# Performance work log

Hardware: AMD Instinct MI355X
Metric: run time of the kernel (lower is better)

The kernel has to match this reference:

```python
import jax, jax.numpy as jnp
import numpy as np

HEADS = 10
HEAD_DIM = 64
ATTN_SCALE = HEAD_DIM ** -0.5
SHARED_SCORE_SHIFT = 0.6931472  # ln(2)
SHARED_SCORE_SCALE = 1.0
EPS = 1e-5


def expand_first(feat, scale=1.0):
    # feat: [b, ...]; broadcast style stats from batch 0 and b//2 over each half
    b = feat.shape[0]
    style = jnp.stack([feat[0], feat[b // 2]])[:, None]          # [2, 1, ...]
    style = jnp.broadcast_to(style, (2, b // 2) + feat.shape[1:])
    if scale != 1.0:
        factors = jnp.where(jnp.arange(b // 2) == 0, 1.0, scale)
        factors = factors.reshape((1, b // 2) + (1,) * (feat.ndim - 1))
        style = style * factors
    return style.reshape(feat.shape)


def adain(feat):
    # stats over the sequence axis (dim=-2); torch .var() is unbiased (ddof=1)
    mean = jnp.mean(feat, axis=-2, keepdims=True)
    std = jnp.sqrt(jnp.var(feat, axis=-2, keepdims=True, ddof=1) + EPS)
    style_mean = expand_first(mean)
    style_std = expand_first(std)
    return (feat - mean) / std * style_std + style_mean


def setup_inputs() -> dict:
    key = jax.random.key(0)
    B, N, C = 4, 2048, 640
    ks = jax.random.split(key, 6)
    hidden_states = jax.random.normal(ks[0], (B, N, C), dtype=jnp.float32)
    w_scale = 0.03
    wq = jax.random.normal(ks[1], (C, C), dtype=jnp.float32) * w_scale
    wk = jax.random.normal(ks[2], (C, C), dtype=jnp.float32) * w_scale
    wv = jax.random.normal(ks[3], (C, C), dtype=jnp.float32) * w_scale
    wo = jax.random.normal(ks[4], (C, C), dtype=jnp.float32) * w_scale
    bo = jnp.zeros((C,), dtype=jnp.float32)
    return {"hidden_states": hidden_states, "wq": wq, "wk": wk, "wv": wv, "wo": wo, "bo": bo}


def reference(hidden_states, wq, wk, wv, wo, bo):
    b, n, c = hidden_states.shape
    # to_q / to_k / to_v (bias-free Linear: y = x @ W^T)
    q = hidden_states @ wq.T
    k = hidden_states @ wk.T
    v = hidden_states @ wv.T
    # [b, heads, n, head_dim]
    q = q.reshape(b, n, HEADS, HEAD_DIM).transpose(0, 2, 1, 3)
    k = k.reshape(b, n, HEADS, HEAD_DIM).transpose(0, 2, 1, 3)
    v = v.reshape(b, n, HEADS, HEAD_DIM).transpose(0, 2, 1, 3)
    # AdaIN on queries and keys (adain_values=False)
    q = adain(q)
    k = adain(k)
    # cross-batch KV style sharing
    k = expand_first(k, SHARED_SCORE_SCALE)
    v = expand_first(v, SHARED_SCORE_SCALE)
    # shifted scaled-dot-product attention: shift added to logit columns >= Nq
    logits = jnp.einsum('bhqd,bhkd->bhqk', q, k) * ATTN_SCALE
    nq, nk = q.shape[2], k.shape[2]
    shift = SHARED_SCORE_SHIFT * (jnp.arange(nk) >= nq).astype(logits.dtype)
    logits = logits + shift  # no-op here since nk == nq, kept for fidelity
    probs = jax.nn.softmax(logits, axis=-1)
    out = jnp.einsum('bhqk,bhkd->bhqd', probs, v)
    # merge heads, output projection (to_out[0] Linear + to_out[1] Dropout=identity)
    out = out.transpose(0, 2, 1, 3).reshape(b, n, HEADS * HEAD_DIM)
    out = out @ wo.T + bo
    # residual connection, rescale_output_factor = 1
    return out + hidden_states
```

## Files before the change

kernel.cpp:

```cpp
#include <hip/hip_runtime.h>
#include <hip/hip_bf16.h>
#include <math.h>

#define Bb 4
#define Nn 2048
#define Cc 640
#define Hh 10
#define Dd 64
#define EPSf 1e-5f
#define QSCALE 0.18033688f
#define KVT 64

typedef __attribute__((ext_vector_type(8))) short bf16x8;
typedef __attribute__((ext_vector_type(4))) float f32x4;
typedef __attribute__((ext_vector_type(16))) float f32x16;
typedef __attribute__((ext_vector_type(8))) unsigned short u16x8;
typedef __attribute__((ext_vector_type(4))) unsigned int u32x4;
typedef __attribute__((ext_vector_type(2))) unsigned int u32x2v;

__device__ inline unsigned short f2bf(float f) {
    unsigned int x = __float_as_uint(f);
    unsigned int r = (x + 0x7fffu + ((x >> 16) & 1u)) >> 16;
    return (unsigned short)r;
}
__device__ inline float bf2f(unsigned short v) {
    return __uint_as_float(((unsigned int)v) << 16);
}
__device__ inline unsigned pkbf(float a, float b) {
    __hip_bfloat162 t = __float22bfloat162_rn(float2{a, b});
    union { __hip_bfloat162 h; unsigned u; } cv; cv.h = t;
    return cv.u;
}
__device__ inline unsigned cvtpk(float lo, float hi) {
    unsigned r;
    asm("v_cvt_pk_bf16_f32 %0, %1, %2" : "=v"(r) : "v"(lo), "v"(hi));
    return r;
}
__device__ inline f32x4 mfma16(bf16x8 a, bf16x8 b, f32x4 c) {
    return __builtin_amdgcn_mfma_f32_16x16x32_bf16(a, b, c, 0, 0, 0);
}
__device__ inline f32x16 mfma32(bf16x8 a, bf16x8 b, f32x16 c) {
    return __builtin_amdgcn_mfma_f32_32x32x16_bf16(a, b, c, 0, 0, 0);
}
__device__ inline void gl16(const ushort* g, char* l) {
    __builtin_amdgcn_global_load_lds(
        (const __attribute__((address_space(1))) unsigned int*)g,
        (__attribute__((address_space(3))) unsigned int*)l, 16, 0, 0);
}

__global__ __launch_bounds__(256)
void tobf16_all(const float* __restrict__ hs, const float* __restrict__ wq,
                const float* __restrict__ wk, const float* __restrict__ wv,
                const float* __restrict__ wo,
                ushort* __restrict__ Xb, ushort* __restrict__ Wqb,
                ushort* __restrict__ Wkb, ushort* __restrict__ Wvb,
                ushort* __restrict__ Wob) {
    const int bid = blockIdx.x;
    const float* src;
    ushort* dst;
    int i;
    if (bid < 2560) {
        src = hs; dst = Xb; i = bid * 256 + threadIdx.x;
    } else {
        int w = (bid - 2560) / 200;
        int rb = (bid - 2560) % 200;
        src = (w == 0) ? wq : (w == 1) ? wk : (w == 2) ? wv : wo;
        dst = (w == 0) ? Wqb : (w == 1) ? Wkb : (w == 2) ? Wvb : Wob;
        i = rb * 256 + threadIdx.x;
    }
    const size_t base = (size_t)i * 8;
    float4 a = *reinterpret_cast<const float4*>(src + base);
    float4 b = *reinterpret_cast<const float4*>(src + base + 4);
    u16x8 o;
    o[0] = f2bf(a.x); o[1] = f2bf(a.y); o[2] = f2bf(a.z); o[3] = f2bf(a.w);
    o[4] = f2bf(b.x); o[5] = f2bf(b.y); o[6] = f2bf(b.z); o[7] = f2bf(b.w);
    *reinterpret_cast<u16x8*>(dst + base) = o;
}

template<int MODE>
__device__ __forceinline__ void gemm_body(
    const ushort* __restrict__ X, const ushort* __restrict__ W,
    ushort* __restrict__ outh, float* __restrict__ outf,
    const float* __restrict__ bo, const ushort* __restrict__ hsb,
    float* __restrict__ Pstats,
    int mt, int h, char* As, char* Bs)
{
    const int tid = threadIdx.x;
    const int wv = tid >> 6, lane = tid & 63;
    const int c = lane & 15, g = lane >> 4;
    const int r0 = mt * 128;
    const int xr0 = (MODE == 1 || MODE == 2) ? (r0 < Nn ? r0 : r0 + Nn) : r0;
    const int o0 = h * 64;

    const int grow = lane >> 3;
    const int gcol = ((((lane & 7) * 16) ^ ((lane >> 3) << 4)) >> 1);

    f32x4 acc[2][4];
    #pragma unroll
    for (int i = 0; i < 2; ++i)
        #pragma unroll
        for (int j = 0; j < 4; ++j)
            acc[i][j] = (f32x4){0.f, 0.f, 0.f, 0.f};

    for (int k0 = 0; k0 < Cc; k0 += 64) {
        __syncthreads();
        #pragma unroll
        for (int i = 0; i < 4; ++i) {
            int a = wv * 4 + i;
            gl16(X + (size_t)(xr0 + a * 8 + grow) * Cc + k0 + gcol, As + a * 1024);
        }
        #pragma unroll
        for (int i = 0; i < 2; ++i) {
            int bb = wv * 2 + i;
            gl16(W + (size_t)(o0 + bb * 8 + grow) * Cc + k0 + gcol, Bs + bb * 1024);
        }
        __syncthreads();

        bf16x8 xf[2][2], wf[4][2];
        #pragma unroll
        for (int rt = 0; rt < 2; ++rt) {
            int row = wv * 32 + rt * 16 + c;
            #pragma unroll
            for (int ks = 0; ks < 2; ++ks)
                xf[rt][ks] = *reinterpret_cast<const bf16x8*>(
                    As + row * 128 + ((ks * 64 + g * 16) ^ ((row & 7) << 4)));
        }
        #pragma unroll
        for (int ct = 0; ct < 4; ++ct) {
            int row = ct * 16 + c;
            #pragma unroll
            for (int ks = 0; ks < 2; ++ks)
                wf[ct][ks] = *reinterpret_cast<const bf16x8*>(
                    Bs + row * 128 + ((ks * 64 + g * 16) ^ ((row & 7) << 4)));
        }
        #pragma unroll
        for (int rt = 0; rt < 2; ++rt)
            #pragma unroll
            for (int ct = 0; ct < 4; ++ct)
                #pragma unroll
                for (int ks = 0; ks < 2; ++ks) {
                    if constexpr (MODE == 2)
                        acc[rt][ct] = mfma16(xf[rt][ks], wf[ct][ks], acc[rt][ct]);
                    else
                        acc[rt][ct] = mfma16(wf[ct][ks], xf[rt][ks], acc[rt][ct]);
                }
    }

    if constexpr (MODE == 0 || MODE == 1) {
        #pragma unroll
        for (int rt = 0; rt < 2; ++rt) {
            int r = r0 + wv * 32 + rt * 16 + c;
            int bi = r >> 11, n = r & 2047;
            #pragma unroll
            for (int ct = 0; ct < 4; ++ct) {
                int d0 = ct * 16 + g * 4;
                ushort4 v4;
                v4.x = f2bf(acc[rt][ct][0]); v4.y = f2bf(acc[rt][ct][1]);
                v4.z = f2bf(acc[rt][ct][2]); v4.w = f2bf(acc[rt][ct][3]);
                *reinterpret_cast<ushort4*>(&outh[(((size_t)(bi * Hh + h)) * Nn + n) * Dd + d0]) = v4;
            }
        }
    } else if constexpr (MODE == 2) {
        #pragma unroll
        for (int rt = 0; rt < 2; ++rt) {
            int r = r0 + wv * 32 + rt * 16 + g * 4;
            int kb = r >> 11, n = r & 2047;
            #pragma unroll
            for (int ct = 0; ct < 4; ++ct) {
                int d = ct * 16 + c;
                ushort4 v4;
                v4.x = f2bf(acc[rt][ct][0]); v4.y = f2bf(acc[rt][ct][1]);
                v4.z = f2bf(acc[rt][ct][2]); v4.w = f2bf(acc[rt][ct][3]);
                *reinterpret_cast<ushort4*>(&outh[(((size_t)(kb * Hh + h)) * Dd + d) * Nn + n]) = v4;
            }
        }
    } else {
        #pragma unroll
        for (int rt = 0; rt < 2; ++rt) {
            int r = r0 + wv * 32 + rt * 16 + c;
            #pragma unroll
            for (int ct = 0; ct < 4; ++ct) {
                int o = h * 64 + ct * 16 + g * 4;
                float4 bvv = *reinterpret_cast<const float4*>(&bo[o]);
                ushort4 hv4 = *reinterpret_cast<const ushort4*>(&hsb[(size_t)r * Cc + o]);
                float4 ov;
                ov.x = acc[rt][ct][0] + bvv.x + bf2f(hv4.x);
                ov.y = acc[rt][ct][1] + bvv.y + bf2f(hv4.y);
                ov.z = acc[rt][ct][2] + bvv.z + bf2f(hv4.z);
                ov.w = acc[rt][ct][3] + bvv.w + bf2f(hv4.w);
                *reinterpret_cast<float4*>(&outf[(size_t)r * Cc + o]) = ov;
            }
        }
    }

    if constexpr (MODE == 0) {
        __syncthreads();
        float* Sw  = (float*)As;
        float* Sw2 = (float*)(As + 1024);
        #pragma unroll
        for (int ct = 0; ct < 4; ++ct) {
            #pragma unroll
            for (int rg = 0; rg < 4; ++rg) {
                float a0 = acc[0][ct][rg], a1 = acc[1][ct][rg];
                float v = a0 + a1;
                float q = a0 * a0 + a1 * a1;
                #pragma unroll
                for (int m = 1; m < 16; m <<= 1) {
                    v += __shfl_xor(v, m);
                    q += __shfl_xor(q, m);
                }
                if (c == 0) {
                    int d = ct * 16 + g * 4 + rg;
                    Sw[wv * 64 + d] = v;
                    Sw2[wv * 64 + d] = q;
                }
            }
        }
        __syncthreads();
        if (tid < 64) {
            float s = Sw[tid] + Sw[64 + tid] + Sw[128 + tid] + Sw[192 + tid];
            float q = Sw2[tid] + Sw2[64 + tid] + Sw2[128 + tid] + Sw2[192 + tid];
            int bi = mt >> 4, slot = mt & 15;
            int bh = bi * Hh + h;
            float* p = Pstats + ((size_t)(bh * 16 + slot) * 2) * 64;
            p[tid] = s;
            p[64 + tid] = q;
        }
    }
}

__global__ __launch_bounds__(256)
void gemm_qkv(const ushort* __restrict__ X, const ushort* __restrict__ Wq,
              const ushort* __restrict__ Wk, const ushort* __restrict__ Wv,
              ushort* __restrict__ Qh, ushort* __restrict__ K16,
              ushort* __restrict__ Vt16, float* __restrict__ Pstats) {
    __shared__ alignas(16) char As[16384];
    __shared__ alignas(16) char Bs[8192];
    const int bx = blockIdx.x;
    if (bx < 64)
        gemm_body<0>(X, Wq, Qh, nullptr, nullptr, nullptr, Pstats, bx, blockIdx.y, As, Bs);
    else if (bx < 96)
        gemm_body<1>(X, Wk, K16, nullptr, nullptr, nullptr, nullptr, bx - 64, blockIdx.y, As, Bs);
    else
        gemm_body<2>(X, Wv, Vt16, nullptr, nullptr, nullptr, nullptr, bx - 96, blockIdx.y, As, Bs);
}

__global__ __launch_bounds__(256)
void gemm_out(const ushort* __restrict__ Ain, const ushort* __restrict__ Wo,
              float* __restrict__ out, const float* __restrict__ bo,
              const ushort* __restrict__ hsb) {
    __shared__ alignas(16) char As[16384];
    __shared__ alignas(16) char Bs[8192];
    gemm_body<3>(Ain, Wo, nullptr, out, bo, hsb, nullptr, blockIdx.x, blockIdx.y, As, Bs);
}

__global__ __launch_bounds__(512, 4)
void attn_mfma(const ushort* __restrict__ Qh, const float* __restrict__ Pstats,
               const ushort* __restrict__ Kb, const ushort* __restrict__ Vtb,
               ushort* __restrict__ Ao) {
    __shared__ alignas(16) char smem[32768];
    __shared__ float lsh[8][32];
    __shared__ float statl[4][64];

    const int tid = threadIdx.x;
    const int wid = tid >> 6, lane = tid & 63;
    const int half = wid >> 2, wq = wid & 3;
    const int q31 = lane & 31, hi = lane >> 5;
    const int bh = blockIdx.x, b = bh / Hh, h = bh % Hh, kb = b >> 1;
    const int qw0 = blockIdx.y * 128 + wq * 32;
    const int kv0 = half * (Nn / 2);

    char* Ksh = smem + half * 8192;
    char* Vsh = smem + 16384 + half * 8192;

    const ushort* qp = Qh + ((size_t)bh * Nn + qw0) * Dd;
    const ushort* kp = Kb + ((size_t)(kb * Hh + h) * Nn + kv0) * Dd;
    const ushort* vp = Vtb + ((size_t)(kb * Hh + h)) * Dd * Nn + kv0;

    if (b & 1) {
        if (tid < 128) {
            const int which = tid >> 6;
            const int d = tid & 63;
            const int tb = which ? (bh - Hh) : bh;
            const float* p = Pstats + ((size_t)(tb * 16) * 2) * 64;
            float s = 0.f, q = 0.f;
            #pragma unroll
            for (int j = 0; j < 16; ++j) {
                s += p[(j * 2) * 64 + d];
                q += p[(j * 2 + 1) * 64 + d];
            }
            float mu = s / (float)Nn;
            float var = (q - (float)Nn * mu * mu) / (float)(Nn - 1);
            float sd = sqrtf(var + EPSf);
            statl[which * 2 + 0][d] = mu;
            statl[which * 2 + 1][d] = sd;
        }
        __syncthreads();
    }

    bf16x8 qf[4];
    #pragma unroll
    for (int dsl = 0; dsl < 4; ++dsl) {
        const int d0 = dsl * 16 + hi * 8;
        u16x8 qin = *reinterpret_cast<const u16x8*>(qp + (size_t)q31 * Dd + d0);
        float x[8];
        #pragma unroll
        for (int j = 0; j < 8; ++j) x[j] = bf2f(qin[j]);
        if (b & 1) {
            #pragma unroll
            for (int j = 0; j < 8; ++j) {
                float r = statl[3][d0 + j] / statl[1][d0 + j];
                x[j] = (x[j] * r + (statl[2][d0 + j] - statl[0][d0 + j] * r)) * QSCALE;
            }
        } else {
            #pragma unroll
            for (int j = 0; j < 8; ++j) x[j] *= QSCALE;
        }
        u32x4 pw = {pkbf(x[0], x[1]), pkbf(x[2], x[3]), pkbf(x[4], x[5]), pkbf(x[6], x[7])};
        qf[dsl] = *reinterpret_cast<bf16x8*>(&pw);
    }

    f32x16 acc0, acc1;
    #pragma unroll
    for (int r = 0; r < 16; ++r) { acc0[r] = 0.f; acc1[r] = 0.f; }
    float l = 0.f;

    const int htid = tid & 255;
    const int srow = htid >> 3, sch = htid & 7;
    const int swz = (sch * 16) ^ ((srow & 7) << 4);
    const int soff0 = srow * 128 + swz;
    const int soff1 = (srow + 32) * 128 + swz;
    const ushort* kg0 = kp + (size_t)srow * Dd + sch * 8;
    const ushort* kg1 = kp + (size_t)(srow + 32) * Dd + sch * 8;
    const ushort* vg0 = vp + (size_t)srow * Nn + sch * 8;
    const ushort* vg1 = vp + (size_t)(srow + 32) * Nn + sch * 8;

    bf16x8 kr0 = *reinterpret_cast<const bf16x8*>(kg0);
    bf16x8 kr1 = *reinterpret_cast<const bf16x8*>(kg1);
    bf16x8 vr0 = *reinterpret_cast<const bf16x8*>(vg0);
    bf16x8 vr1 = *reinterpret_cast<const bf16x8*>(vg1);
    *reinterpret_cast<bf16x8*>(Ksh + soff0) = kr0;
    *reinterpret_cast<bf16x8*>(Ksh + soff1) = kr1;
    *reinterpret_cast<bf16x8*>(Vsh + soff0) = vr0;
    *reinterpret_cast<bf16x8*>(Vsh + soff1) = vr1;
    __syncthreads();

    const int kx = (q31 & 7) << 4;

    for (int kt = 0; kt < Nn / 2; kt += KVT) {
        const bool has_next = (kt + KVT) < (Nn / 2);
        if (has_next) {
            kr0 = *reinterpret_cast<const bf16x8*>(kg0 + (size_t)(kt + KVT) * Dd);
            kr1 = *reinterpret_cast<const bf16x8*>(kg1 + (size_t)(kt + KVT) * Dd);
            vr0 = *reinterpret_cast<const bf16x8*>(vg0 + kt + KVT);
            vr1 = *reinterpret_cast<const bf16x8*>(vg1 + kt + KVT);
        }

        f32x16 st0, st1;
        #pragma unroll
        for (int r = 0; r < 16; ++r) { st0[r] = 0.f; st1[r] = 0.f; }
        #pragma unroll
        for (int dsl = 0; dsl < 4; ++dsl) {
            bf16x8 kf0 = *reinterpret_cast<const bf16x8*>(
                Ksh + q31 * 128 + ((dsl * 32 + hi * 16) ^ kx));
            bf16x8 kf1 = *reinterpret_cast<const bf16x8*>(
                Ksh + (q31 + 32) * 128 + ((dsl * 32 + hi * 16) ^ kx));
            st0 = mfma32(kf0, qf[dsl], st0);
            st1 = mfma32(kf1, qf[dsl], st1);
        }

        #pragma unroll
        for (int r = 0; r < 16; ++r) st0[r] = __builtin_amdgcn_exp2f(st0[r]);
        #pragma unroll
        for (int r = 0; r < 16; ++r) st1[r] = __builtin_amdgcn_exp2f(st1[r]);

        {
            float s2[16];
            #pragma unroll
            for (int r = 0; r < 16; ++r) s2[r] = st0[r] + st1[r];
            float s4[8];
            #pragma unroll
            for (int r = 0; r < 8; ++r) s4[r] = s2[r] + s2[r + 8];
            float s8[4];
            #pragma unroll
            for (int r = 0; r < 4; ++r) s8[r] = s4[r] + s4[r + 4];
            l += (s8[0] + s8[1]) + (s8[2] + s8[3]);
        }

        #pragma unroll
        for (int kvm = 0; kvm < 2; ++kvm) {
            #pragma unroll
            for (int tt = 0; tt < 2; ++tt) {
                float p0, p1, p2, p3, p4, p5, p6, p7;
                if (kvm == 0) {
                    p0 = st0[8*tt+0]; p1 = st0[8*tt+1]; p2 = st0[8*tt+2]; p3 = st0[8*tt+3];
                    p4 = st0[8*tt+4]; p5 = st0[8*tt+5]; p6 = st0[8*tt+6]; p7 = st0[8*tt+7];
                } else {
                    p0 = st1[8*tt+0]; p1 = st1[8*tt+1]; p2 = st1[8*tt+2]; p3 = st1[8*tt+3];
                    p4 = st1[8*tt+4]; p5 = st1[8*tt+5]; p6 = st1[8*tt+6]; p7 = st1[8*tt+7];
                }
                unsigned a0 = cvtpk(p0, p1);
                unsigned a1 = cvtpk(p2, p3);
                unsigned b0 = cvtpk(p4, p5);
                unsigned b1 = cvtpk(p6, p7);
                u32x2v r0 = __builtin_amdgcn_permlane32_swap(a0, b0, false, false);
                u32x2v r1 = __builtin_amdgcn_permlane32_swap(a1, b1, false, false);
                u32x4 fw = {r0[0], r1[0], r0[1], r1[1]};
                bf16x8 pf = *reinterpret_cast<bf16x8*>(&fw);
                const int km = kvm * 2 + tt;
                bf16x8 vf0 = *reinterpret_cast<const bf16x8*>(
                    Vsh + q31 * 128 + ((km * 32 + hi * 16) ^ kx));
                bf16x8 vf1 = *reinterpret_cast<const bf16x8*>(
                    Vsh + (q31 + 32) * 128 + ((km * 32 + hi * 16) ^ kx));
                acc0 = mfma32(pf, vf0, acc0);
                acc1 = mfma32(pf, vf1, acc1);
            }
        }

        if (has_next) {
            __syncthreads();
            *reinterpret_cast<bf16x8*>(Ksh + soff0) = kr0;
            *reinterpret_cast<bf16x8*>(Ksh + soff1) = kr1;
            *reinterpret_cast<bf16x8*>(Vsh + soff0) = vr0;
            *reinterpret_cast<bf16x8*>(Vsh + soff1) = vr1;
            __syncthreads();
        }
    }

    l += __shfl_xor(l, 32);
    lsh[wid][q31] = l;
    __syncthreads();
    float* fs = (float*)smem;
    if (half == 1) {
        float* dst = fs + wq * 2048;
        #pragma unroll
        for (int r = 0; r < 16; ++r) {
            dst[r * 64 + lane] = acc0[r];
            dst[(16 + r) * 64 + lane] = acc1[r];
        }
    }
    __syncthreads();
    if (half == 0) {
        const float* src = fs + wq * 2048;
        float ltot = l + lsh[wid + 4][q31];
        float inv = 1.0f / ltot;
        #pragma unroll
        for (int r = 0; r < 16; ++r) {
            const int qlr = (r & 3) + 8 * (r >> 2) + 4 * hi;
            float o0 = (acc0[r] + src[r * 64 + lane]) * inv;
            float o1 = (acc1[r] + src[(16 + r) * 64 + lane]) * inv;
            size_t o = (size_t)(b * Nn + qw0 + qlr) * Cc + h * Dd + q31;
            Ao[o]      = f2bf(o0);
            Ao[o + 32] = f2bf(o1);
        }
    }
}

extern "C" void kernel_launch(void* const* d_in, const int* in_sizes, int n_in,
                              void* d_out, int out_size, void* d_ws, size_t ws_size,
                              hipStream_t stream) {
    const float* hs = (const float*)d_in[0];
    const float* wq = (const float*)d_in[1];
    const float* wk = (const float*)d_in[2];
    const float* wv = (const float*)d_in[3];
    const float* wo = (const float*)d_in[4];
    const float* bo = (const float*)d_in[5];
    float* out = (float*)d_out;

    ushort* Xb   = (ushort*)d_ws;
    ushort* Wqb  = Xb + 5242880;
    ushort* Wkb  = Wqb + 409600;
    ushort* Wvb  = Wkb + 409600;
    ushort* Wob  = Wvb + 409600;
    ushort* Qh   = Wob + 409600;
    ushort* K16  = Qh + 5242880;
    ushort* Vt16 = K16 + 2621440;
    ushort* Aob  = Vt16 + 2621440;
    float*  Pstats = (float*)(Aob + 5242880);

    tobf16_all<<<3360, 256, 0, stream>>>(hs, wq, wk, wv, wo, Xb, Wqb, Wkb, Wvb, Wob);

    gemm_qkv<<<dim3(128, 10), 256, 0, stream>>>(Xb, Wqb, Wkb, Wvb, Qh, K16, Vt16, Pstats);
    attn_mfma<<<dim3(40, 16), 512, 0, stream>>>(Qh, Pstats, K16, Vt16, Aob);
    gemm_out<<<dim3(64, 10), 256, 0, stream>>>(Aob, Wob, out, bo, Xb);
}
```

Baseline: 117.3 us.

## Double-buffer attention K/V tiles with direct global-to-LDS loads

Replaces the register-staged K/V prefetch in the attention kernel with a double-buffered LDS scheme that issues direct global-to-LDS loads (gl16) for the next tile while the current tile is computed. This cuts the per-iteration barriers from two to one and frees the registers that held the prefetched tiles. In exchange the kernel's shared memory doubles to 64 KB, which may limit how many blocks fit per CU under launch_bounds(512,4).

```diff
diff --git a/kernel.cpp b/kernel.cpp
--- a/kernel.cpp
+++ b/kernel.cpp
@@ -258,20 +258,18 @@
 void attn_mfma(const ushort* __restrict__ Qh, const float* __restrict__ Pstats,
                const ushort* __restrict__ Kb, const ushort* __restrict__ Vtb,
                ushort* __restrict__ Ao) {
-    __shared__ alignas(16) char smem[32768];
+    __shared__ alignas(16) char smem[65536];
     __shared__ float lsh[8][32];
     __shared__ float statl[4][64];
 
     const int tid = threadIdx.x;
     const int wid = tid >> 6, lane = tid & 63;
     const int half = wid >> 2, wq = wid & 3;
+    const int hw = wid & 3;
     const int q31 = lane & 31, hi = lane >> 5;
     const int bh = blockIdx.x, b = bh / Hh, h = bh % Hh, kb = b >> 1;
     const int qw0 = blockIdx.y * 128 + wq * 32;
     const int kv0 = half * (Nn / 2);
-
-    char* Ksh = smem + half * 8192;
-    char* Vsh = smem + 16384 + half * 8192;
 
     const ushort* qp = Qh + ((size_t)bh * Nn + qw0) * Dd;
     const ushort* kp = Kb + ((size_t)(kb * Hh + h) * Nn + kv0) * Dd;
@@ -325,36 +323,32 @@
     for (int r = 0; r < 16; ++r) { acc0[r] = 0.f; acc1[r] = 0.f; }
     float l = 0.f;
 
-    const int htid = tid & 255;
-    const int srow = htid >> 3, sch = htid & 7;
-    const int swz = (sch * 16) ^ ((srow & 7) << 4);
-    const int soff0 = srow * 128 + swz;
-    const int soff1 = (srow + 32) * 128 + swz;
-    const ushort* kg0 = kp + (size_t)srow * Dd + sch * 8;
-    const ushort* kg1 = kp + (size_t)(srow + 32) * Dd + sch * 8;
-    const ushort* vg0 = vp + (size_t)srow * Nn + sch * 8;
-    const ushort* vg1 = vp + (size_t)(srow + 32) * Nn + sch * 8;
-
-    bf16x8 kr0 = *reinterpret_cast<const bf16x8*>(kg0);
-    bf16x8 kr1 = *reinterpret_cast<const bf16x8*>(kg1);
-    bf16x8 vr0 = *reinterpret_cast<const bf16x8*>(vg0);
-    bf16x8 vr1 = *reinterpret_cast<const bf16x8*>(vg1);
-    *reinterpret_cast<bf16x8*>(Ksh + soff0) = kr0;
-    *reinterpret_cast<bf16x8*>(Ksh + soff1) = kr1;
-    *reinterpret_cast<bf16x8*>(Vsh + soff0) = vr0;
-    *reinterpret_cast<bf16x8*>(Vsh + soff1) = vr1;
+    const int grow = lane >> 3;
+    const int gcolE = ((((lane & 7) * 16) ^ ((lane >> 3) << 4)) >> 1);
+
+    auto stage = [&](int kt0, char* buf) {
+        #pragma unroll
+        for (int i = 0; i < 2; ++i) {
+            int blk = hw * 2 + i;
+            gl16(kp + (size_t)(kt0 + blk * 8 + grow) * Dd + gcolE,
+                 buf + half * 8192 + blk * 1024);
+            gl16(vp + (size_t)(blk * 8 + grow) * Nn + kt0 + gcolE,
+                 buf + 16384 + half * 8192 + blk * 1024);
+        }
+    };
+
+    stage(0, smem);
     __syncthreads();
 
     const int kx = (q31 & 7) << 4;
+    unsigned boff = 0;
 
     for (int kt = 0; kt < Nn / 2; kt += KVT) {
         const bool has_next = (kt + KVT) < (Nn / 2);
-        if (has_next) {
-            kr0 = *reinterpret_cast<const bf16x8*>(kg0 + (size_t)(kt + KVT) * Dd);
-            kr1 = *reinterpret_cast<const bf16x8*>(kg1 + (size_t)(kt + KVT) * Dd);
-            vr0 = *reinterpret_cast<const bf16x8*>(vg0 + kt + KVT);
-            vr1 = *reinterpret_cast<const bf16x8*>(vg1 + kt + KVT);
-        }
+        char* buf = smem + boff;
+        if (has_next) stage(kt + KVT, smem + (boff ^ 32768u));
+        char* Ksh = buf + half * 8192;
+        char* Vsh = buf + 16384 + half * 8192;
 
         f32x16 st0, st1;
         #pragma unroll
@@ -417,14 +411,8 @@
             }
         }
 
-        if (has_next) {
-            __syncthreads();
-            *reinterpret_cast<bf16x8*>(Ksh + soff0) = kr0;
-            *reinterpret_cast<bf16x8*>(Ksh + soff1) = kr1;
-            *reinterpret_cast<bf16x8*>(Vsh + soff0) = vr0;
-            *reinterpret_cast<bf16x8*>(Vsh + soff1) = vr1;
-            __syncthreads();
-        }
+        __syncthreads();
+        boff ^= 32768u;
     }
 
     l += __shfl_xor(l, 32);
```

Measured after the change: 118.8 us. Within noise of the previous version (+1.3%).
